# Performance work log

Measured on AMD Instinct MI355X. Metric: run time of the kernel, lower is better.

The kernel has to match this reference:

```python
import jax, jax.numpy as jnp
import numpy as np

N = 100000
E = 1600000
F_IN = 3
H = 64


def setup_inputs() -> dict:
    key = jax.random.key(0)
    ks = jax.random.split(key, 12)
    x = jax.random.normal(ks[0], (N, F_IN), dtype=jnp.float32)
    edge_index = jax.random.randint(ks[1], (2, E), 0, N, dtype=jnp.int64)
    def glorot(k, fi, fo):
        s = jnp.sqrt(6.0 / (fi + fo)).astype(jnp.float32)
        return jax.random.uniform(k, (fi, fo), jnp.float32, -s, s)
    return {
        "x": x,
        "edge_index": edge_index,
        "W1": glorot(ks[2], F_IN, H), "b1": jnp.zeros((H,), jnp.float32),
        "W2": glorot(ks[3], H, H),   "b2": jnp.zeros((H,), jnp.float32),
        "W3": glorot(ks[4], H, H),   "b3": jnp.zeros((H,), jnp.float32),
        "Wh": glorot(ks[5], H, 1),   "bh": jnp.zeros((1,), jnp.float32),
    }


def _gcn_conv(x, src, dst, norm, W, b):
    # linear (no bias) -> gather by src -> scale by symmetric norm -> scatter-add to dst -> + bias
    h = x @ W                      # [N, F_out]
    msg = h[src] * norm[:, None]   # [E+N, F_out] (self-loops included)
    out = jax.ops.segment_sum(msg, dst, num_segments=N)
    return out + b


def reference(x, edge_index, W1, b1, W2, b2, W3, b3, Wh, bh):
    # add self-loops (PyG GCNConv default)
    loop = jnp.arange(N, dtype=edge_index.dtype)
    src = jnp.concatenate([edge_index[0], loop])
    dst = jnp.concatenate([edge_index[1], loop])
    # symmetric normalization deg^{-1/2}[src] * deg^{-1/2}[dst]
    deg = jax.ops.segment_sum(jnp.ones_like(dst, dtype=x.dtype), dst, num_segments=N)
    dinv = jnp.where(deg > 0, jax.lax.rsqrt(deg), 0.0)
    norm = dinv[src] * dinv[dst]

    h = _gcn_conv(x, src, dst, norm, W1, b1)
    h = jax.nn.relu(h)  # dropout is identity in eval mode
    h = _gcn_conv(h, src, dst, norm, W2, b2)
    h = jax.nn.relu(h)
    h = _gcn_conv(h, src, dst, norm, W3, b3)
    logits = (h @ Wh + bh).squeeze(-1)  # [N]
    return logits
```

## Files before the change

kernel.cpp:

```cpp
#include <hip/hip_runtime.h>


#define BKSH 8
#define EPB  4096

__device__ __forceinline__ float rlane(float v, int l) {
    return __int_as_float(__builtin_amdgcn_readlane(__float_as_int(v), l));
}
__device__ __forceinline__ int rlane_i(int v, int l) {
    return __builtin_amdgcn_readlane(v, l);
}

__global__ void bhist(const int* __restrict__ dst, int* __restrict__ ghist,
                      int E, int NBK, int BLK) {
    __shared__ int h[512];
    int t = threadIdx.x, b = blockIdx.x;
    for (int i = t; i < NBK; i += 256) h[i] = 0;
    __syncthreads();
    int base = b * EPB;
    #pragma unroll
    for (int i = 0; i < 16; ++i) {
        int e = base + i * 256 + t;
        if (e < E) atomicAdd(&h[dst[e] >> BKSH], 1);
    }
    __syncthreads();
    for (int i = t; i < NBK; i += 256) ghist[(size_t)i * BLK + b] = h[i];
}

__global__ void gscan1(const int* __restrict__ in, int* __restrict__ out,
                       int* __restrict__ bsums, int M) {
    __shared__ int tmp[256];
    int i = blockIdx.x * 256 + threadIdx.x;
    int v = (i < M) ? in[i] : 0;
    tmp[threadIdx.x] = v; __syncthreads();
    for (int off = 1; off < 256; off <<= 1) {
        int t = (threadIdx.x >= off) ? tmp[threadIdx.x - off] : 0;
        __syncthreads();
        tmp[threadIdx.x] += t;
        __syncthreads();
    }
    if (i < M) out[i] = tmp[threadIdx.x] - v;
    if (threadIdx.x == 255) bsums[blockIdx.x] = tmp[255];
}

__global__ void gscan2(int* __restrict__ bsums, int nb) {
    __shared__ int tmp[1024];
    int v = (threadIdx.x < nb) ? bsums[threadIdx.x] : 0;
    tmp[threadIdx.x] = v; __syncthreads();
    for (int off = 1; off < 1024; off <<= 1) {
        int t = (threadIdx.x >= off) ? tmp[threadIdx.x - off] : 0;
        __syncthreads();
        tmp[threadIdx.x] += t;
        __syncthreads();
    }
    if (threadIdx.x < nb) bsums[threadIdx.x] = tmp[threadIdx.x] - v;
}

__global__ void bscatter(const int* __restrict__ src, const int* __restrict__ dst,
                         const int* __restrict__ goff, const int* __restrict__ gbsums,
                         unsigned* __restrict__ tmp, int E, int NBK, int BLK) {
    __shared__ int off[512];
    int t = threadIdx.x, b = blockIdx.x;
    for (int i = t; i < NBK; i += 256) {
        size_t m = (size_t)i * BLK + b;
        off[i] = goff[m] + gbsums[m >> 8];
    }
    __syncthreads();
    int base = b * EPB;
    #pragma unroll
    for (int i = 0; i < 16; ++i) {
        int e = base + i * 256 + t;
        if (e < E) {
            int d = dst[e];
            int p = atomicAdd(&off[d >> BKSH], 1);
            tmp[p] = ((unsigned)src[e] << 8) | (unsigned)(d & 255);
        }
    }
}

__global__ void bucketAF(const unsigned* __restrict__ tmp, const int* __restrict__ goff,
                         const int* __restrict__ gbsums, const float* __restrict__ x,
                         int* __restrict__ rowptr, float* __restrict__ dinv,
                         float4* __restrict__ xd4, int* __restrict__ ewsrc,
                         int N, int NBK, int BLK, int E) {
    __shared__ int lc[256], sc[256], rbase[256];
    int b = blockIdx.x, t = threadIdx.x;
    lc[t] = 0; __syncthreads();
    size_t m0 = (size_t)b * BLK;
    int p0 = goff[m0] + gbsums[m0 >> 8];
    int p1 = E;
    if (b + 1 < NBK) { size_t m1 = (size_t)(b + 1) * BLK; p1 = goff[m1] + gbsums[m1 >> 8]; }
    for (int p = p0 + t; p < p1; p += 256) atomicAdd(&lc[tmp[p] & 255u], 1);
    __syncthreads();
    int v = lc[t];
    sc[t] = v; __syncthreads();
    for (int off = 1; off < 256; off <<= 1) {
        int tv = (t >= off) ? sc[t - off] : 0;
        __syncthreads();
        sc[t] += tv;
        __syncthreads();
    }
    int rb = p0 + (sc[t] - v);
    rbase[t] = rb;
    int node = (b << BKSH) + t;
    if (node < N) {
        rowptr[node] = rb;
        float dvv = rsqrtf((float)(v + 1));
        dinv[node] = dvv;
        xd4[node]  = make_float4(dvv * x[3*node], dvv * x[3*node+1],
                                 dvv * x[3*node+2], 0.f);
    }
    if (b == 0 && t == 0) rowptr[N] = E;
    lc[t] = 0;
    __syncthreads();
    for (int p = p0 + t; p < p1; p += 256) {
        unsigned e = tmp[p];
        int dl = (int)(e & 255u);
        int pos = rbase[dl] + atomicAdd(&lc[dl], 1);
        ewsrc[pos] = (int)(e >> 8);
    }
}

__global__ void agg3w(const int* __restrict__ ewsrc, const int* __restrict__ rowptr,
                      const float* __restrict__ dinv, const float4* __restrict__ xd4,
                      float4* __restrict__ a1, int N) {
    int g   = (blockIdx.x * blockDim.x + threadIdx.x) >> 4;
    int sub = threadIdx.x & 15;
    if (g >= N) return;
    int p0 = rowptr[g], p1 = rowptr[g+1];
    float ax = 0.f, ay = 0.f, az = 0.f;
    for (int p = p0 + sub; p < p1; p += 16) {
        float4 xs = xd4[ewsrc[p]];
        ax += xs.x; ay += xs.y; az += xs.z;
    }
    #pragma unroll
    for (int off = 8; off; off >>= 1) {
        ax += __shfl_down(ax, off, 16);
        ay += __shfl_down(ay, off, 16);
        az += __shfl_down(az, off, 16);
    }
    if (sub == 0) {
        float dv = dinv[g];
        float4 xn = xd4[g];
        a1[g] = make_float4(dv * (ax + xn.x), dv * (ay + xn.y),
                            dv * (az + xn.z), dv);
    }
}

__global__ void fold_head(const float* __restrict__ W3, const float* __restrict__ b3,
                          const float* __restrict__ Wh, const float* __restrict__ bh,
                          float* __restrict__ wc) {
    int k = threadIdx.x;
    float acc = 0.0f;
    for (int f = 0; f < 64; f++) acc += W3[k*64+f] * Wh[f];
    wc[k] = acc;
    if (k == 0) {
        float bb = bh[0];
        for (int f = 0; f < 64; f++) bb += b3[f] * Wh[f];
        wc[64] = bb;
    }
}

__global__ void fused_l2l3(const int* __restrict__ ewsrc, const int* __restrict__ rowptr,
                           const float4* __restrict__ a1, const float* __restrict__ W1,
                           const float* __restrict__ b1, const float* __restrict__ W2,
                           const float* __restrict__ b2, const float* __restrict__ wc,
                           float* __restrict__ zz, int N, int E) {
    __shared__ float  Wl[64*64];
    __shared__ float4 pay[4][64];
    __shared__ float  a2buf[4][64];
    const int tid = threadIdx.x;
    for (int i = tid; i < 4096; i += 256) Wl[i] = W2[i];
    const int lane = tid & 63;
    const int wv   = tid >> 6;
    const float w10 = W1[lane], w11 = W1[64+lane], w12 = W1[128+lane];
    const float b1f = b1[lane], b2f = b2[lane], wcf = wc[lane];
    const int NPW = 8;
    const int n0 = (blockIdx.x * 4 + wv) * NPW;
    int   rpl = rowptr[min(n0 + lane, N)];
    float4 sg = a1[min(n0 + lane, N - 1)];
    __syncthreads();
    if (n0 >= N) return;
    int NPWv = N - n0; if (NPWv > NPW) NPWv = NPW;
    int p0c = rlane_i(rpl, 0), p1c = rlane_i(rpl, 1);
    float4 g_c = make_float4(0.f, 0.f, 0.f, 0.f);
    if (p0c < p1c) {
        int pidx = p0c + lane; if (pidx >= p1c) pidx = p1c - 1;
        g_c = a1[ewsrc[pidx]];
    }
    for (int cur = 0; cur < NPWv; ++cur) {
        int p0 = p0c, p1 = p1c;
        pay[wv][lane] = g_c;
        if (cur + 1 < NPWv) {
            p0c = rlane_i(rpl, cur + 1);
            p1c = rlane_i(rpl, cur + 2);
            if (p0c < p1c) {
                int pidx = p0c + lane; if (pidx >= p1c) pidx = p1c - 1;
                g_c = a1[ewsrc[pidx]];
            }
        }
        float sx = rlane(sg.x, cur), sy = rlane(sg.y, cur);
        float sz2 = rlane(sg.z, cur), sw = rlane(sg.w, cur);
        float ts = fmaf(sz2, w12, fmaf(sy, w11, fmaf(sx, w10, b1f)));
        float acc0 = sw * fmaxf(ts, 0.f);
        float acc1 = 0.f, acc2 = 0.f, acc3 = 0.f;
        {
            int m = p1 - p0; if (m > 64) m = 64;
            const float4* pp = (const float4*)&pay[wv][0];
            int j = 0;
            for (; j + 3 < m; j += 4) {
                float4 P0 = pp[j], P1 = pp[j+1], P2 = pp[j+2], P3 = pp[j+3];
                float t0 = fmaf(P0.z, w12, fmaf(P0.y, w11, fmaf(P0.x, w10, b1f)));
                float t1 = fmaf(P1.z, w12, fmaf(P1.y, w11, fmaf(P1.x, w10, b1f)));
                float t2 = fmaf(P2.z, w12, fmaf(P2.y, w11, fmaf(P2.x, w10, b1f)));
                float t3 = fmaf(P3.z, w12, fmaf(P3.y, w11, fmaf(P3.x, w10, b1f)));
                acc0 = fmaf(P0.w, fmaxf(t0, 0.f), acc0);
                acc1 = fmaf(P1.w, fmaxf(t1, 0.f), acc1);
                acc2 = fmaf(P2.w, fmaxf(t2, 0.f), acc2);
                acc3 = fmaf(P3.w, fmaxf(t3, 0.f), acc3);
            }
            for (; j < m; ++j) {
                float4 P = pp[j];
                float tt = fmaf(P.z, w12, fmaf(P.y, w11, fmaf(P.x, w10, b1f)));
                acc1 = fmaf(P.w, fmaxf(tt, 0.f), acc1);
            }
        }
        for (int pc = p0 + 64; pc < p1; pc += 64) {
            int pidx = pc + lane; if (pidx >= p1) pidx = p1 - 1;
            float4 g2 = a1[ewsrc[pidx]];
            pay[wv][lane] = g2;
            int m2 = p1 - pc; if (m2 > 64) m2 = 64;
            const float4* pp = (const float4*)&pay[wv][0];
            for (int j = 0; j < m2; ++j) {
                float4 P = pp[j];
                float tt = fmaf(P.z, w12, fmaf(P.y, w11, fmaf(P.x, w10, b1f)));
                acc2 = fmaf(P.w, fmaxf(tt, 0.f), acc2);
            }
        }
        float acc = ((acc0 + acc1) + (acc2 + acc3)) * sw;
        a2buf[wv][lane] = acc;
        float ha = 0.f, hb = 0.f, hc = 0.f, hd = 0.f;
        const float4* a4 = (const float4*)&a2buf[wv][0];
        #pragma unroll
        for (int k4 = 0; k4 < 16; ++k4) {
            float4 a = a4[k4];
            ha = fmaf(a.x, Wl[(4*k4+0)*64 + lane], ha);
            hb = fmaf(a.y, Wl[(4*k4+1)*64 + lane], hb);
            hc = fmaf(a.z, Wl[(4*k4+2)*64 + lane], hc);
            hd = fmaf(a.w, Wl[(4*k4+3)*64 + lane], hd);
        }
        float h = b2f + ((ha + hb) + (hc + hd));
        float v = fmaxf(h, 0.f) * wcf;
        #pragma unroll
        for (int off = 32; off; off >>= 1) v += __shfl_down(v, off);
        if (lane == 0) zz[n0 + cur] = sw * v;
    }
}

__global__ void final_wave(const float* __restrict__ zz, const int* __restrict__ ewsrc,
                           const int* __restrict__ rowptr, const float* __restrict__ dinv,
                           const float* __restrict__ wc, float* __restrict__ out, int N) {
    int g   = (blockIdx.x * blockDim.x + threadIdx.x) >> 4;
    int sub = threadIdx.x & 15;
    if (g >= N) return;
    int p0 = rowptr[g], p1 = rowptr[g+1];
    float acc = 0.f;
    for (int p = p0 + sub; p < p1; p += 16) {
        acc += zz[ewsrc[p]];
    }
    #pragma unroll
    for (int off = 8; off; off >>= 1) acc += __shfl_down(acc, off, 16);
    if (sub == 0) {
        out[g] = fmaf(dinv[g], zz[g] + acc, wc[64]);
    }
}

extern "C" void kernel_launch(void* const* d_in, const int* in_sizes, int n_in,
                              void* d_out, int out_size, void* d_ws, size_t ws_size,
                              hipStream_t stream) {
    const float* x   = (const float*)d_in[0];
    const int*   ei  = (const int*)d_in[1];
    const float* W1  = (const float*)d_in[2];
    const float* b1  = (const float*)d_in[3];
    const float* W2  = (const float*)d_in[4];
    const float* b2  = (const float*)d_in[5];
    const float* W3  = (const float*)d_in[6];
    const float* b3  = (const float*)d_in[7];
    const float* Wh  = (const float*)d_in[8];
    const float* bh  = (const float*)d_in[9];
    float* logits = (float*)d_out;

    const int N = in_sizes[0] / 3;
    const int E = in_sizes[1] / 2;
    const int* src = ei;
    const int* dst = ei + E;

    const int NBK = (N + 255) >> BKSH;
    const int BLK = (E + EPB - 1) / EPB;
    const int M   = NBK * BLK;

    float* base = (float*)d_ws;
    size_t o = 0;
    float*    dinv   = base + o; o += (size_t)N;
    o = (o + 3) & ~(size_t)3;
    float4*   a1     = (float4*)(base + o); o += (size_t)4*N;
    float4*   xd4    = (float4*)(base + o); o += (size_t)4*N;
    int*      rowptr = (int*)(base + o); o += (size_t)N + 1;
    int*      gbsums = (int*)(base + o); o += 1024;
    int*      ewsrc  = (int*)(base + o); o += (size_t)E;
    unsigned* tmpp   = (unsigned*)(base + o); o += (size_t)E;
    float*    zz     = base + o; o += (size_t)N;
    float*    wc     = base + o; o += 65;
    int*      ghist  = (int*)(base + o); o += (size_t)M;
    int*      goff   = (int*)(base + o); o += (size_t)M;

    const int BS = 256;
    int gM   = (M + BS - 1) / BS;
    int g16  = ((size_t)N * 16 + BS - 1) / BS;
    int gFU  = (N + 31) / 32;

    bhist    <<<BLK, BS, 0, stream>>>(dst, ghist, E, NBK, BLK);
    gscan1   <<<gM,  BS, 0, stream>>>(ghist, goff, gbsums, M);
    gscan2   <<<1, 1024, 0, stream>>>(gbsums, gM);
    bscatter <<<BLK, BS, 0, stream>>>(src, dst, goff, gbsums, tmpp, E, NBK, BLK);
    bucketAF <<<NBK, BS, 0, stream>>>(tmpp, goff, gbsums, x, rowptr, dinv, xd4, ewsrc, N, NBK, BLK, E);
    agg3w    <<<g16, BS, 0, stream>>>(ewsrc, rowptr, dinv, xd4, a1, N);

    fold_head  <<<1, 64, 0, stream>>>(W3, b3, Wh, bh, wc);
    fused_l2l3 <<<gFU, BS, 0, stream>>>(ewsrc, rowptr, a1, W1, b1, W2, b2, wc, zz, N, E);
    final_wave <<<g16, BS, 0, stream>>>(zz, ewsrc, rowptr, dinv, wc, logits, N);
}
```

Before: 139.6 us.

## Batch-stage neighbor payloads for a wave's nodes and fold head into agg3w

The fused layer-2/3 kernel now gathers the neighbor payloads for all eight of a wave's nodes at once into a larger shared buffer (up to 192 entries), instead of prefetching one node at a time. The per-node inner loop then reads its slice of the staged buffer, and any nodes past the cap fall back to chunked gathers. The tiny fold_head kernel is merged into agg3w's first block, removing one launch. The larger shared-memory footprint per block (about 12KB of payload instead of 4KB) may reduce occupancy, and the gather no longer overlaps with compute on the previous node.

```diff
diff --git a/kernel.cpp b/kernel.cpp
--- a/kernel.cpp
+++ b/kernel.cpp
@@ -3,6 +3,7 @@
 
 #define BKSH 8
 #define EPB  4096
+#define PAYCAP 192
 
 __device__ __forceinline__ float rlane(float v, int l) {
     return __int_as_float(__builtin_amdgcn_readlane(__float_as_int(v), l));
@@ -123,7 +124,21 @@
 
 __global__ void agg3w(const int* __restrict__ ewsrc, const int* __restrict__ rowptr,
                       const float* __restrict__ dinv, const float4* __restrict__ xd4,
-                      float4* __restrict__ a1, int N) {
+                      float4* __restrict__ a1,
+                      const float* __restrict__ W3, const float* __restrict__ b3,
+                      const float* __restrict__ Wh, const float* __restrict__ bh,
+                      float* __restrict__ wc, int N) {
+    if (blockIdx.x == 0 && threadIdx.x < 64) {
+        int k = threadIdx.x;
+        float accw = 0.f;
+        for (int f = 0; f < 64; f++) accw += W3[k*64+f] * Wh[f];
+        wc[k] = accw;
+        if (k == 0) {
+            float bb = bh[0];
+            for (int f = 0; f < 64; f++) bb += b3[f] * Wh[f];
+            wc[64] = bb;
+        }
+    }
     int g   = (blockIdx.x * blockDim.x + threadIdx.x) >> 4;
     int sub = threadIdx.x & 15;
     if (g >= N) return;
@@ -147,27 +162,13 @@
     }
 }
 
-__global__ void fold_head(const float* __restrict__ W3, const float* __restrict__ b3,
-                          const float* __restrict__ Wh, const float* __restrict__ bh,
-                          float* __restrict__ wc) {
-    int k = threadIdx.x;
-    float acc = 0.0f;
-    for (int f = 0; f < 64; f++) acc += W3[k*64+f] * Wh[f];
-    wc[k] = acc;
-    if (k == 0) {
-        float bb = bh[0];
-        for (int f = 0; f < 64; f++) bb += b3[f] * Wh[f];
-        wc[64] = bb;
-    }
-}
-
 __global__ void fused_l2l3(const int* __restrict__ ewsrc, const int* __restrict__ rowptr,
                            const float4* __restrict__ a1, const float* __restrict__ W1,
                            const float* __restrict__ b1, const float* __restrict__ W2,
                            const float* __restrict__ b2, const float* __restrict__ wc,
                            float* __restrict__ zz, int N, int E) {
     __shared__ float  Wl[64*64];
-    __shared__ float4 pay[4][64];
+    __shared__ float4 pay[4][PAYCAP];
     __shared__ float  a2buf[4][64];
     const int tid = threadIdx.x;
     for (int i = tid; i < 4096; i += 256) Wl[i] = W2[i];
@@ -182,59 +183,55 @@
     __syncthreads();
     if (n0 >= N) return;
     int NPWv = N - n0; if (NPWv > NPW) NPWv = NPW;
-    int p0c = rlane_i(rpl, 0), p1c = rlane_i(rpl, 1);
-    float4 g_c = make_float4(0.f, 0.f, 0.f, 0.f);
-    if (p0c < p1c) {
-        int pidx = p0c + lane; if (pidx >= p1c) pidx = p1c - 1;
-        g_c = a1[ewsrc[pidx]];
+    const int P0 = rlane_i(rpl, 0);
+    const int P8 = rlane_i(rpl, NPWv);
+    int span  = P8 - P0;
+    int stage = span < PAYCAP ? span : PAYCAP;
+    for (int w = 0; w < stage; w += 64) {
+        int idx = w + lane;
+        if (idx < stage) pay[wv][idx] = a1[ewsrc[P0 + idx]];
     }
     for (int cur = 0; cur < NPWv; ++cur) {
-        int p0 = p0c, p1 = p1c;
-        pay[wv][lane] = g_c;
-        if (cur + 1 < NPWv) {
-            p0c = rlane_i(rpl, cur + 1);
-            p1c = rlane_i(rpl, cur + 2);
-            if (p0c < p1c) {
-                int pidx = p0c + lane; if (pidx >= p1c) pidx = p1c - 1;
-                g_c = a1[ewsrc[pidx]];
-            }
-        }
+        int p0 = rlane_i(rpl, cur);
+        int p1 = rlane_i(rpl, cur + 1);
         float sx = rlane(sg.x, cur), sy = rlane(sg.y, cur);
         float sz2 = rlane(sg.z, cur), sw = rlane(sg.w, cur);
         float ts = fmaf(sz2, w12, fmaf(sy, w11, fmaf(sx, w10, b1f)));
         float acc0 = sw * fmaxf(ts, 0.f);
         float acc1 = 0.f, acc2 = 0.f, acc3 = 0.f;
         {
-            int m = p1 - p0; if (m > 64) m = 64;
+            int js  = p0 - P0;
+            int jse = p1 - P0; if (jse > stage) jse = stage;
             const float4* pp = (const float4*)&pay[wv][0];
-            int j = 0;
-            for (; j + 3 < m; j += 4) {
-                float4 P0 = pp[j], P1 = pp[j+1], P2 = pp[j+2], P3 = pp[j+3];
-                float t0 = fmaf(P0.z, w12, fmaf(P0.y, w11, fmaf(P0.x, w10, b1f)));
-                float t1 = fmaf(P1.z, w12, fmaf(P1.y, w11, fmaf(P1.x, w10, b1f)));
-                float t2 = fmaf(P2.z, w12, fmaf(P2.y, w11, fmaf(P2.x, w10, b1f)));
-                float t3 = fmaf(P3.z, w12, fmaf(P3.y, w11, fmaf(P3.x, w10, b1f)));
-                acc0 = fmaf(P0.w, fmaxf(t0, 0.f), acc0);
-                acc1 = fmaf(P1.w, fmaxf(t1, 0.f), acc1);
-                acc2 = fmaf(P2.w, fmaxf(t2, 0.f), acc2);
-                acc3 = fmaf(P3.w, fmaxf(t3, 0.f), acc3);
+            int j = js;
+            for (; j + 3 < jse; j += 4) {
+                float4 Q0 = pp[j], Q1 = pp[j+1], Q2 = pp[j+2], Q3 = pp[j+3];
+                float t0 = fmaf(Q0.z, w12, fmaf(Q0.y, w11, fmaf(Q0.x, w10, b1f)));
+                float t1 = fmaf(Q1.z, w12, fmaf(Q1.y, w11, fmaf(Q1.x, w10, b1f)));
+                float t2 = fmaf(Q2.z, w12, fmaf(Q2.y, w11, fmaf(Q2.x, w10, b1f)));
+                float t3 = fmaf(Q3.z, w12, fmaf(Q3.y, w11, fmaf(Q3.x, w10, b1f)));
+                acc0 = fmaf(Q0.w, fmaxf(t0, 0.f), acc0);
+                acc1 = fmaf(Q1.w, fmaxf(t1, 0.f), acc1);
+                acc2 = fmaf(Q2.w, fmaxf(t2, 0.f), acc2);
+                acc3 = fmaf(Q3.w, fmaxf(t3, 0.f), acc3);
             }
-            for (; j < m; ++j) {
-                float4 P = pp[j];
-                float tt = fmaf(P.z, w12, fmaf(P.y, w11, fmaf(P.x, w10, b1f)));
-                acc1 = fmaf(P.w, fmaxf(tt, 0.f), acc1);
+            for (; j < jse; ++j) {
+                float4 Q = pp[j];
+                float tt = fmaf(Q.z, w12, fmaf(Q.y, w11, fmaf(Q.x, w10, b1f)));
+                acc1 = fmaf(Q.w, fmaxf(tt, 0.f), acc1);
             }
         }
-        for (int pc = p0 + 64; pc < p1; pc += 64) {
+        int ov = P0 + stage; if (ov < p0) ov = p0;
+        for (int pc = ov; pc < p1; pc += 64) {
             int pidx = pc + lane; if (pidx >= p1) pidx = p1 - 1;
             float4 g2 = a1[ewsrc[pidx]];
             pay[wv][lane] = g2;
             int m2 = p1 - pc; if (m2 > 64) m2 = 64;
             const float4* pp = (const float4*)&pay[wv][0];
-            for (int j = 0; j < m2; ++j) {
-                float4 P = pp[j];
-                float tt = fmaf(P.z, w12, fmaf(P.y, w11, fmaf(P.x, w10, b1f)));
-                acc2 = fmaf(P.w, fmaxf(tt, 0.f), acc2);
+            for (int jj = 0; jj < m2; ++jj) {
+                float4 Q = pp[jj];
+                float tt = fmaf(Q.z, w12, fmaf(Q.y, w11, fmaf(Q.x, w10, b1f)));
+                acc2 = fmaf(Q.w, fmaxf(tt, 0.f), acc2);
             }
         }
         float acc = ((acc0 + acc1) + (acc2 + acc3)) * sw;
@@ -324,9 +321,8 @@
     gscan2   <<<1, 1024, 0, stream>>>(gbsums, gM);
     bscatter <<<BLK, BS, 0, stream>>>(src, dst, goff, gbsums, tmpp, E, NBK, BLK);
     bucketAF <<<NBK, BS, 0, stream>>>(tmpp, goff, gbsums, x, rowptr, dinv, xd4, ewsrc, N, NBK, BLK, E);
-    agg3w    <<<g16, BS, 0, stream>>>(ewsrc, rowptr, dinv, xd4, a1, N);
-
-    fold_head  <<<1, 64, 0, stream>>>(W3, b3, Wh, bh, wc);
+    agg3w    <<<g16, BS, 0, stream>>>(ewsrc, rowptr, dinv, xd4, a1, W3, b3, Wh, bh, wc, N);
+
     fused_l2l3 <<<gFU, BS, 0, stream>>>(ewsrc, rowptr, a1, W1, b1, W2, b2, wc, zz, N, E);
     final_wave <<<g16, BS, 0, stream>>>(zz, ewsrc, rowptr, dinv, wc, logits, N);
 }
```

New measurement: 132.2 us, median of 2. 5.3% less time.
